# Performance work log

Measured on AMD Instinct MI355X. Metric: run time of the kernel, lower is better.

## Reference

```python
import jax, jax.numpy as jnp
import numpy as np

P, Q, B = 256, 48, 16      # passage len, question len, batch
E, H = 300, 128            # word embed size, hidden size
D = E + 2 * H              # preprocess GRU input dim (word emb + bidir char emb)


def _gru_layer(xs, Wih, Whh, bih, bhh):
    """torch.nn.GRU single layer over time. xs: [T,B,in] -> [T,B,H]."""
    def step(h, x):
        gi = x @ Wih.T + bih
        gh = h @ Whh.T + bhh
        ir, iz, inn = jnp.split(gi, 3, axis=-1)
        hr, hz, hn = jnp.split(gh, 3, axis=-1)
        r = jax.nn.sigmoid(ir + hr)
        z = jax.nn.sigmoid(iz + hz)
        n = jnp.tanh(inn + r * hn)
        h2 = (1.0 - z) * n + z * h
        return h2, h2
    h0 = jnp.zeros((xs.shape[1], Whh.shape[-1]), xs.dtype)
    return jax.lax.scan(step, h0, xs)[1]


def _lstm_cell(x, h, c, Wih, Whh, b):
    """torch.nn.LSTMCell gate order i,f,g,o."""
    g = x @ Wih.T + h @ Whh.T + b
    i, f, gg, o = jnp.split(g, 4, axis=-1)
    c2 = jax.nn.sigmoid(f) * c + jax.nn.sigmoid(i) * jnp.tanh(gg)
    return jax.nn.sigmoid(o) * jnp.tanh(c2), c2


def _preprocess(x, gru):
    """3-layer GRU run on forward and time-reversed input (shared weights), concat -> [T,B,2H]."""
    def run(xs):
        h = xs
        for (Wih, Whh, bih, bhh) in gru:
            h = _gru_layer(h, Wih, Whh, bih, bhh)
        return h
    Hf = run(x)
    Hb = jnp.flip(run(jnp.flip(x, 0)), 0)
    return jnp.concatenate([Hf, Hb], axis=-1)


def _bidir_attn_lstm(Hseq, Hmem, Wmem, Wcur, Whid, w_att, Wg, Wih, Whh, b):
    """Gated additive-attention LSTM (match-LSTM / self-matching) run in both
    directions over Hseq with a shared cell, attending over Hmem. -> [T,B,2H]."""
    att_mem = jnp.einsum('qbd,hd->qbh', Hmem, Wmem)          # [Tm,B,H], precomputed
    def step(carry, x_t):
        h, c = carry
        g = jnp.tanh(att_mem + x_t @ Wcur.T + h @ Whid.T)    # [Tm,B,H]
        a = jax.nn.softmax(jnp.einsum('qbh,h->qb', g, w_att), axis=0)
        w = jnp.einsum('qb,qbd->bd', a, Hmem)                # [B,2H]
        z = jnp.concatenate([x_t, w], axis=-1)               # [B,4H]
        z = z * jax.nn.sigmoid(z @ Wg.T)                     # gated attention input
        h, c = _lstm_cell(z, h, c, Wih, Whh, b)
        return (h, c), h
    z0 = jnp.zeros((Hseq.shape[1], Whh.shape[-1]), Hseq.dtype)
    Hf = jax.lax.scan(step, (z0, z0), Hseq)[1]
    Hb = jax.lax.scan(step, (z0, z0), jnp.flip(Hseq, 0))[1]
    return jnp.concatenate([Hf, jnp.flip(Hb, 0)], axis=-1)


def _forward(p_inp, q_inp, g0_Wih, g0_Whh, g0_bih, g0_bhh, g1_Wih, g1_Whh, g1_bih, g1_bhh, g2_Wih, g2_Whh, g2_bih, g2_bhh, Wq, Wp, Wh, w_alpha, Wg_m, m_Wih, m_Whh, m_b, Wsp, Wsh, w_gamma, Wg_s, s_Wih, s_Whh, s_b, Wal, Waa, w_beta, Wah, bah, Wac, bac, pt_Wih, pt_Whh, pt_b):
    gru = [(g0_Wih, g0_Whh, g0_bih, g0_bhh),
           (g1_Wih, g1_Whh, g1_bih, g1_bhh),
           (g2_Wih, g2_Whh, g2_bih, g2_bhh)]
    Hp = _preprocess(p_inp, gru)                             # [P,B,2H]
    Hq = _preprocess(q_inp, gru)                             # [Q,B,2H]
    # gated match-LSTM: passage attends over question
    Hr = _bidir_attn_lstm(Hp, Hq, Wq, Wp, Wh, w_alpha, Wg_m, m_Wih, m_Whh, m_b)
    # gated self-matching: passage attends over itself (shared attend_self_passage)
    Hs = _bidir_attn_lstm(Hr, Hr, Wsp, Wsp, Wsh, w_gamma, Wg_s, s_Wih, s_Whh, s_b)
    # answer pointer network, init state from pooled question representation
    qp = Hq.mean(axis=0)                                     # [B,2H]
    h = qp @ Wah.T + bah
    c = qp @ Wac.T + bac
    att = jnp.einsum('pbd,hd->pbh', Hs, Wal)                 # [P,B,H]
    betas = []
    for _ in range(2):                                       # start / end pointer steps
        g = jnp.tanh(att + h @ Waa.T)
        beta = jax.nn.softmax(jnp.einsum('pbh,h->pb', g, w_beta), axis=0)
        betas.append(beta)
        wv = jnp.einsum('pb,pbd->bd', beta, Hs)              # [B,2H]
        h, c = _lstm_cell(wv, h, c, pt_Wih, pt_Whh, pt_b)
    return jnp.stack(betas)                                  # [2,P,B]


def setup_inputs() -> dict:
    ks = iter(jax.random.split(jax.random.key(0), 64))
    def rn(shape, s=0.08):
        return jax.random.normal(next(ks), shape, jnp.float32) * s
    d = {}
    d['p_inp'] = jax.random.normal(next(ks), (P, B, D), jnp.float32)
    d['q_inp'] = jax.random.normal(next(ks), (Q, B, D), jnp.float32)
    for i, ind in enumerate([D, H, H]):
        d['g%d_Wih' % i] = rn((3 * H, ind))
        d['g%d_Whh' % i] = rn((3 * H, H))
        d['g%d_bih' % i] = jnp.zeros((3 * H,), jnp.float32)
        d['g%d_bhh' % i] = jnp.zeros((3 * H,), jnp.float32)
    d['Wq'] = rn((H, 2 * H)); d['Wp'] = rn((H, 2 * H)); d['Wh'] = rn((H, H))
    d['w_alpha'] = rn((H,))
    d['Wg_m'] = rn((4 * H, 4 * H))
    d['m_Wih'] = rn((4 * H, 4 * H)); d['m_Whh'] = rn((4 * H, H)); d['m_b'] = jnp.zeros((4 * H,), jnp.float32)
    d['Wsp'] = rn((H, 2 * H)); d['Wsh'] = rn((H, H)); d['w_gamma'] = rn((H,))
    d['Wg_s'] = rn((4 * H, 4 * H))
    d['s_Wih'] = rn((4 * H, 4 * H)); d['s_Whh'] = rn((4 * H, H)); d['s_b'] = jnp.zeros((4 * H,), jnp.float32)
    d['Wal'] = rn((H, 2 * H)); d['Waa'] = rn((H, H)); d['w_beta'] = rn((H,))
    d['Wah'] = rn((H, 2 * H)); d['bah'] = jnp.zeros((H,), jnp.float32)
    d['Wac'] = rn((H, 2 * H)); d['bac'] = jnp.zeros((H,), jnp.float32)
    d['pt_Wih'] = rn((4 * H, 2 * H)); d['pt_Whh'] = rn((4 * H, H)); d['pt_b'] = jnp.zeros((4 * H,), jnp.float32)
    return d


def reference(p_inp, q_inp, g0_Wih, g0_Whh, g0_bih, g0_bhh, g1_Wih, g1_Whh, g1_bih, g1_bhh, g2_Wih, g2_Whh, g2_bih, g2_bhh, Wq, Wp, Wh, w_alpha, Wg_m, m_Wih, m_Whh, m_b, Wsp, Wsh, w_gamma, Wg_s, s_Wih, s_Whh, s_b, Wal, Waa, w_beta, Wah, bah, Wac, bac, pt_Wih, pt_Whh, pt_b):
    return _forward(p_inp, q_inp, g0_Wih, g0_Whh, g0_bih, g0_bhh, g1_Wih, g1_Whh, g1_bih, g1_bhh, g2_Wih, g2_Whh, g2_bih, g2_bhh, Wq, Wp, Wh, w_alpha, Wg_m, m_Wih, m_Whh, m_b, Wsp, Wsh, w_gamma, Wg_s, s_Wih, s_Whh, s_b, Wal, Waa, w_beta, Wah, bah, Wac, bac, pt_Wih, pt_Whh, pt_b)
```

## Files before the change

kernel.cpp:

```cpp
#include <hip/hip_runtime.h>


#define PP 256
#define QQ 48
#define BB 16

typedef _Float16 f16;
typedef f16 f16x4 __attribute__((ext_vector_type(4)));
typedef f16 f16x8 __attribute__((ext_vector_type(8)));
typedef f16 h2 __attribute__((ext_vector_type(2)));

__device__ __forceinline__ float fast_rcp(float x) { return __builtin_amdgcn_rcpf(x); }
__device__ __forceinline__ float tanh_f(float x) {
  float e = __expf(2.0f * x);
  return 1.0f - 2.0f * fast_rcp(1.0f + e);
}
__device__ __forceinline__ float sigm_f(float x) {
  return fast_rcp(1.0f + __expf(-x));
}
__device__ __forceinline__ float fdot2(h2 a, h2 b, float c) {
#if defined(__has_builtin)
#if __has_builtin(__builtin_amdgcn_fdot2)
  return __builtin_amdgcn_fdot2(a, b, c, false);
#else
  return c + (float)a.x*(float)b.x + (float)a.y*(float)b.y;
#endif
#else
  return c + (float)a.x*(float)b.x + (float)a.y*(float)b.y;
#endif
}

__global__ __launch_bounds__(256) void gemm_nt(
    const float* __restrict__ A, int lda,
    const float* __restrict__ W, int ldw,
    const float* __restrict__ bias,
    float* __restrict__ C, int ldc, int K) {
  __shared__ float As[64][17];
  __shared__ float Ws[64][17];
  int tid = threadIdx.x;
  int m0 = blockIdx.x * 64, n0 = blockIdx.y * 64;
  int lr = tid >> 2, lq = (tid & 3) * 4;
  int tr = tid >> 4, tc = tid & 15;
  float acc[4][4] = {};
  for (int k0 = 0; k0 < K; k0 += 16) {
    float4 av = {0,0,0,0}, wv = {0,0,0,0};
    if (k0 + lq < K) {
      av = *(const float4*)&A[(size_t)(m0 + lr) * lda + k0 + lq];
      wv = *(const float4*)&W[(size_t)(n0 + lr) * ldw + k0 + lq];
    }
    __syncthreads();
    As[lr][lq+0] = av.x; As[lr][lq+1] = av.y; As[lr][lq+2] = av.z; As[lr][lq+3] = av.w;
    Ws[lr][lq+0] = wv.x; Ws[lr][lq+1] = wv.y; Ws[lr][lq+2] = wv.z; Ws[lr][lq+3] = wv.w;
    __syncthreads();
#pragma unroll
    for (int kk = 0; kk < 16; ++kk) {
      float a4[4], b4[4];
#pragma unroll
      for (int i = 0; i < 4; ++i) a4[i] = As[tr*4+i][kk];
#pragma unroll
      for (int j = 0; j < 4; ++j) b4[j] = Ws[tc*4+j][kk];
#pragma unroll
      for (int i = 0; i < 4; ++i)
#pragma unroll
        for (int j = 0; j < 4; ++j) acc[i][j] += a4[i] * b4[j];
    }
  }
#pragma unroll
  for (int i = 0; i < 4; ++i) {
    int m = m0 + tr*4 + i;
#pragma unroll
    for (int j = 0; j < 4; ++j) {
      int n = n0 + tc*4 + j;
      C[(size_t)m * ldc + n] = acc[i][j] + (bias ? bias[n] : 0.0f);
    }
  }
}

__global__ __launch_bounds__(256) void gemm_f16u(
    const float* __restrict__ A, int lda,
    const float* __restrict__ W, int ldw,
    f16* __restrict__ dst, int QMd, int K) {
  __shared__ float As[64][17];
  __shared__ float Ws[64][17];
  int tid = threadIdx.x;
  int m0 = blockIdx.x * 64, n0 = blockIdx.y * 64;
  int lr = tid >> 2, lq = (tid & 3) * 4;
  int tr = tid >> 4, tc = tid & 15;
  float acc[4][4] = {};
  for (int k0 = 0; k0 < K; k0 += 16) {
    float4 av = *(const float4*)&A[(size_t)(m0 + lr) * lda + k0 + lq];
    float4 wv = *(const float4*)&W[(size_t)(n0 + lr) * ldw + k0 + lq];
    __syncthreads();
    As[lr][lq+0] = av.x; As[lr][lq+1] = av.y; As[lr][lq+2] = av.z; As[lr][lq+3] = av.w;
    Ws[lr][lq+0] = wv.x; Ws[lr][lq+1] = wv.y; Ws[lr][lq+2] = wv.z; Ws[lr][lq+3] = wv.w;
    __syncthreads();
#pragma unroll
    for (int kk = 0; kk < 16; ++kk) {
      float a4[4], b4[4];
#pragma unroll
      for (int i = 0; i < 4; ++i) a4[i] = As[tr*4+i][kk];
#pragma unroll
      for (int j = 0; j < 4; ++j) b4[j] = Ws[tc*4+j][kk];
#pragma unroll
      for (int i = 0; i < 4; ++i)
#pragma unroll
        for (int j = 0; j < 4; ++j) acc[i][j] += a4[i] * b4[j];
    }
  }
#pragma unroll
  for (int i = 0; i < 4; ++i) {
    int m = m0 + tr*4 + i;
    int q = m >> 4, bb = m & 15;
#pragma unroll
    for (int j = 0; j < 4; ++j) {
      int n = n0 + tc*4 + j;
      dst[((size_t)bb*QMd + q)*768 + 256 + n] = (f16)acc[i][j];
    }
  }
}

__global__ void conv_hmemU(const float* __restrict__ src, f16* __restrict__ dst, int QM) {
  int q = blockIdx.x, b = blockIdx.y, d = threadIdx.x;
  dst[((size_t)b*QM + q)*768 + d] = (f16)src[((size_t)q*BB + b)*256 + d];
}

struct TDesc { const float* src; float* dst; int R, C, ld, off; };
struct TDescs { TDesc d[5]; };

__global__ __launch_bounds__(256) void transpose_many(TDescs ds) {
  TDesc d = ds.d[blockIdx.y];
  int idx = blockIdx.x * 256 + threadIdx.x;
  if (idx < d.R * d.C) {
    int r = idx / d.C, cc = idx % d.C;
    d.dst[(size_t)cc * d.R + r] = d.src[(size_t)r * d.ld + d.off + cc];
  }
}

struct HDesc { const float* src; f16* dst; int R, C, ld; };
struct HDescs { HDesc d[7]; };

__global__ __launch_bounds__(256) void conv_w16_many(HDescs ds) {
  HDesc d = ds.d[blockIdx.y];
  int idx = blockIdx.x * 256 + threadIdx.x;
  if (idx < d.R * d.C) {
    int j = idx / d.C, k = idx % d.C;
    d.dst[(size_t)k * d.R + j] = (f16)d.src[(size_t)j * d.ld + k];
  }
}

struct QDesc { const float* src; h2* dst; int J, K, ld; };
struct QDescs { QDesc d[2]; };

__global__ __launch_bounds__(256) void pack_pairs_many(QDescs ds) {
  QDesc d = ds.d[blockIdx.y];
  int KP = d.K >> 1;
  int idx = blockIdx.x * 256 + threadIdx.x;
  if (idx < KP * d.J) {
    int kp = idx / d.J, j = idx % d.J;
    h2 v;
    v.x = (f16)d.src[(size_t)j*d.ld + 2*kp];
    v.y = (f16)d.src[(size_t)j*d.ld + 2*kp + 1];
    d.dst[(size_t)kp*d.J + j] = v;
  }
}

__global__ __launch_bounds__(256) void conv_attT(
    const float* __restrict__ src, f16* __restrict__ dst, int QM) {
  int idx = blockIdx.x * 256 + threadIdx.x;
  if (idx < 16*128*QM) {
    int q = idx % QM, h = (idx / QM) & 127, b = idx / (QM*128);
    dst[idx] = (f16)src[((size_t)q*BB + b)*128 + h];
  }
}

__global__ __launch_bounds__(512) void gru_rec(
    const float* __restrict__ gi_p, const float* __restrict__ gi_q,
    const f16* __restrict__ WhhH,
    const float* __restrict__ bhh,
    float* __restrict__ out_p, float* __restrict__ out_q,
    float* __restrict__ Hp, float* __restrict__ Hq,
    int mode0, int finalmode) {
  int x = blockIdx.x;
  int seq = x >> 3, dir = (x >> 2) & 1, bg = x & 3;
  int T = seq ? QQ : PP;
  const float* gi = seq ? gi_q : gi_p;
  float* out = seq ? out_q : out_p;
  float* Hf  = seq ? Hq   : Hp;
  int b0 = bg * 4;
  int tid = threadIdx.x;
  __shared__ float hs[4][128];
  __shared__ float gpart[4][4][384];
  ((float*)hs)[tid] = 0.0f;
  __syncthreads();
  int ks = tid / 96;
  int jq = (tid % 96) * 4;
  int gb = tid >> 7, gj = tid & 127;
  for (int t = 0; t < T; ++t) {
    if (tid < 384) {
      float a[4][4] = {};
      const f16* wp = WhhH + (size_t)ks*32*384 + jq;
      const int kb = ks*32;
#pragma unroll 8
      for (int k = 0; k < 32; ++k) {
        f16x4 wv = *(const f16x4*)&wp[(size_t)k*384];
        float w0 = (float)wv[0], w1 = (float)wv[1], w2 = (float)wv[2], w3 = (float)wv[3];
#pragma unroll
        for (int bb = 0; bb < 4; ++bb) {
          float hv = hs[bb][kb + k];
          a[bb][0] += hv*w0; a[bb][1] += hv*w1; a[bb][2] += hv*w2; a[bb][3] += hv*w3;
        }
      }
#pragma unroll
      for (int bb = 0; bb < 4; ++bb) {
        gpart[ks][bb][jq+0]=a[bb][0]; gpart[ks][bb][jq+1]=a[bb][1];
        gpart[ks][bb][jq+2]=a[bb][2]; gpart[ks][bb][jq+3]=a[bb][3];
      }
    }
    __syncthreads();
    {
      size_t base;
      if (mode0) {
        int girow = dir ? (T-1-t) : t;
        base = ((size_t)girow*BB + b0+gb)*384;
      } else {
        base = (((size_t)dir*T + t)*BB + b0+gb)*384;
      }
      float ghr = bhh[gj]     + gpart[0][gb][gj]     + gpart[1][gb][gj]     + gpart[2][gb][gj]     + gpart[3][gb][gj];
      float ghz = bhh[128+gj] + gpart[0][gb][128+gj] + gpart[1][gb][128+gj] + gpart[2][gb][128+gj] + gpart[3][gb][128+gj];
      float ghn = bhh[256+gj] + gpart[0][gb][256+gj] + gpart[1][gb][256+gj] + gpart[2][gb][256+gj] + gpart[3][gb][256+gj];
      float gr = gi[base + gj], gz = gi[base + 128 + gj], gn = gi[base + 256 + gj];
      float r = sigm_f(gr + ghr);
      float z = sigm_f(gz + ghz);
      float n = tanh_f(gn + r * ghn);
      float h2v = (1.0f - z) * n + z * hs[gb][gj];
      hs[gb][gj] = h2v;
      if (finalmode) {
        int orow = dir ? (T-1-t) : t;
        Hf[((size_t)orow*BB + b0+gb)*256 + dir*128 + gj] = h2v;
      } else {
        out[(((size_t)dir*T + t)*BB + b0+gb)*128 + gj] = h2v;
      }
    }
    __syncthreads();
  }
}

template<int QM>
__global__ __launch_bounds__(512) void attn_rec2(
    const float* __restrict__ Hseq,
    const f16*  __restrict__ HmemU,
    const f16*  __restrict__ attT,
    const float* __restrict__ Xcur,
    const float* __restrict__ Xg,
    const float* __restrict__ watt,
    const f16*  __restrict__ WhidT,
    const h2*   __restrict__ WihP2,
    const f16*  __restrict__ WhhT,
    const float* __restrict__ bias,
    float* __restrict__ Hy) {
  constexpr bool HOST = (QM == QQ);
  constexpr int QP  = HOST ? 64 : 256;
  constexpr int HS  = 512 / QP;
  constexpr int hl  = 128 / HS;
  constexpr int hsh = HOST ? 6 : 8;
  constexpr int QR  = QM / 4;
  int dir = blockIdx.x >> 4, b = blockIdx.x & 15;
  int tid = threadIdx.x;
  __shared__ f16 attSL[HOST ? 128*QQ : 1];
  __shared__ f16 humSL[HOST ? QQ*768 : 1];
  __shared__ float h[128], c[128], xh[128], wa[128];
  __shared__ float peS[QP], zx[256];
  __shared__ h2 zgP[256];
  __shared__ float pA[4][128];
  __shared__ float pB[512];
  __shared__ float pDE[4][768];
  __shared__ float pG[8][512];
  __shared__ float biasS[512];
  __shared__ float red[1];
  if (tid < 128) { h[tid] = 0.0f; c[tid] = 0.0f; wa[tid] = watt[tid]; }
  biasS[tid] = bias[tid];
  const f16* attb = attT  + (size_t)b*128*QM;
  const f16* humb = HmemU + (size_t)b*QM*768;
  if constexpr (HOST) {
    for (int i = tid; i < QQ*768/8; i += 512)
      *(f16x8*)&humSL[i*8] = *(const f16x8*)&humb[(size_t)i*8];
    for (int i = tid; i < 128*QQ/8; i += 512)
      *(f16x8*)&attSL[i*8] = *(const f16x8*)&attb[(size_t)i*8];
  }
  __syncthreads();
  for (int t = 0; t < PP; ++t) {
    int row = dir ? (PP-1-t) : t;
    {
      int j = tid & 127, kh = tid >> 7;
      float acc = 0.0f;
      const f16* wp = WhidT + (size_t)kh*32*128 + j;
      const float* hp = &h[kh*32];
#pragma unroll
      for (int k = 0; k < 32; ++k) acc += (float)wp[(size_t)k*128] * hp[k];
      pA[kh][j] = acc;
      if (tid < 128) xh[tid] = Xcur[((size_t)row*BB + b)*128 + tid];
      else if (tid < 192) *(float4*)&zx[(tid-128)*4] =
          *(const float4*)&Hseq[((size_t)row*BB + b)*256 + (tid-128)*4];
    }
    __syncthreads();
    {
      int q = tid & (QP-1), hh = tid >> hsh;
      float acc = 0.0f;
      if (q < QM) {
        const f16* ap = (HOST ? attSL : attb) + q;
        int h0 = hh * hl;
#pragma unroll 8
        for (int i = 0; i < hl; ++i) {
          int h2i = h0 + i;
          float xv = xh[h2i] + pA[0][h2i] + pA[1][h2i] + pA[2][h2i] + pA[3][h2i];
          acc += wa[h2i] * tanh_f((float)ap[(size_t)h2i*QM] + xv);
        }
      }
      pB[hh*QP + q] = acc;
    }
    __syncthreads();
    if (tid < 64) {
      float lsum = 0.0f;
      for (int q2 = tid; q2 < QP; q2 += 64) {
        float s = 0.0f;
#pragma unroll
        for (int i = 0; i < HS; ++i) s += pB[i*QP + q2];
        float e = (q2 < QM) ? __expf(s) : 0.0f;
        peS[q2] = e; lsum += e;
      }
#pragma unroll
      for (int off = 32; off; off >>= 1) lsum += __shfl_down(lsum, off);
      if (tid == 0) red[0] = lsum;
    }
    __syncthreads();
    {
      int oc = tid & 127, qs = tid >> 7;
      if (oc < 96) {
        float a[8] = {};
        if constexpr (HOST) {
          const f16* hp = &humSL[(size_t)(qs*QR)*768 + oc*8];
#pragma unroll
          for (int i = 0; i < QR; ++i) {
            float pv = peS[qs*QR + i];
            f16x8 mv = *(const f16x8*)&hp[(size_t)i*768];
#pragma unroll
            for (int cN = 0; cN < 8; ++cN) a[cN] += pv * (float)mv[cN];
          }
        } else {
          const f16* hp = humb + (size_t)(qs*QR)*768 + oc*8;
#pragma unroll 16
          for (int i = 0; i < QR; ++i) {
            float pv = peS[qs*QR + i];
            f16x8 mv = *(const f16x8*)&hp[(size_t)i*768];
#pragma unroll
            for (int cN = 0; cN < 8; ++cN) a[cN] += pv * (float)mv[cN];
          }
        }
#pragma unroll
        for (int cN = 0; cN < 8; ++cN) pDE[qs][oc*8 + cN] = a[cN];
      }
    }
    __syncthreads();
    if (tid < 256) {
      float invd = fast_rcp(red[0]);
      int j0 = 2*tid;
      float u0 = (pDE[0][256+j0] + pDE[1][256+j0] + pDE[2][256+j0] + pDE[3][256+j0]) * invd;
      float u1 = (pDE[0][257+j0] + pDE[1][257+j0] + pDE[2][257+j0] + pDE[3][257+j0]) * invd;
      float z0, z1;
      if (tid < 128) { z0 = zx[j0]; z1 = zx[j0+1]; }
      else {
        int d0 = j0 - 256;
        z0 = (pDE[0][d0]   + pDE[1][d0]   + pDE[2][d0]   + pDE[3][d0])   * invd;
        z1 = (pDE[0][d0+1] + pDE[1][d0+1] + pDE[2][d0+1] + pDE[3][d0+1]) * invd;
      }
      float2 xg2 = *(const float2*)&Xg[((size_t)row*BB + b)*512 + j0];
      h2 p;
      p.x = (f16)(z0 * sigm_f(xg2.x + u0));
      p.y = (f16)(z1 * sigm_f(xg2.y + u1));
      zgP[tid] = p;
    }
    __syncthreads();
    {
      int jo = tid & 63, kh = tid >> 6;
      float a[8] = {};
      const h2* wp = WihP2 + (size_t)(kh*32)*512 + jo*8;
#pragma unroll 16
      for (int kp = 0; kp < 32; ++kp) {
        const f16* w8 = (const f16*)(wp + (size_t)kp*512);
        f16x8 wlo = *(const f16x8*)w8;
        f16x8 whi = *(const f16x8*)(w8 + 8);
        h2 zv = zgP[kh*32 + kp];
        h2 p0; p0.x = wlo[0]; p0.y = wlo[1];
        h2 p1; p1.x = wlo[2]; p1.y = wlo[3];
        h2 p2; p2.x = wlo[4]; p2.y = wlo[5];
        h2 p3; p3.x = wlo[6]; p3.y = wlo[7];
        h2 p4; p4.x = whi[0]; p4.y = whi[1];
        h2 p5; p5.x = whi[2]; p5.y = whi[3];
        h2 p6; p6.x = whi[4]; p6.y = whi[5];
        h2 p7; p7.x = whi[6]; p7.y = whi[7];
        a[0] = fdot2(p0, zv, a[0]); a[1] = fdot2(p1, zv, a[1]);
        a[2] = fdot2(p2, zv, a[2]); a[3] = fdot2(p3, zv, a[3]);
        a[4] = fdot2(p4, zv, a[4]); a[5] = fdot2(p5, zv, a[5]);
        a[6] = fdot2(p6, zv, a[6]); a[7] = fdot2(p7, zv, a[7]);
      }
      const f16* wp2 = WhhT + (size_t)(kh*16)*512 + jo*8;
      const float* hp = &h[kh*16];
#pragma unroll
      for (int k = 0; k < 16; ++k) {
        float hk = hp[k];
        f16x8 wv = *(const f16x8*)&wp2[(size_t)k*512];
#pragma unroll
        for (int cN = 0; cN < 8; ++cN) a[cN] += hk * (float)wv[cN];
      }
#pragma unroll
      for (int cN = 0; cN < 8; ++cN) pG[kh][jo*8 + cN] = a[cN];
    }
    __syncthreads();
    if (tid < 128) {
      float gi2 = biasS[tid], gf2 = biasS[128+tid], gg2 = biasS[256+tid], go2 = biasS[384+tid];
#pragma unroll
      for (int s = 0; s < 8; ++s) {
        gi2 += pG[s][tid];       gf2 += pG[s][128+tid];
        gg2 += pG[s][256+tid];   go2 += pG[s][384+tid];
      }
      float ii = sigm_f(gi2), ff = sigm_f(gf2), gg = tanh_f(gg2), oo = sigm_f(go2);
      float cn = ff * c[tid] + ii * gg;
      float hn = oo * tanh_f(cn);
      c[tid] = cn; h[tid] = hn;
      Hy[((size_t)row*BB + b)*256 + dir*128 + tid] = hn;
    }
    __syncthreads();
  }
}

__global__ __launch_bounds__(256) void ptr_net(
    const float* __restrict__ Hq,
    const float* __restrict__ Hs,
    const float* __restrict__ attp,
    const float* __restrict__ WaaT,
    const float* __restrict__ wbeta,
    const float* __restrict__ WahT,
    const float* __restrict__ bah,
    const float* __restrict__ WacT,
    const float* __restrict__ bac,
    const float* __restrict__ WihT,
    const float* __restrict__ WhhT,
    const float* __restrict__ bptr,
    float* __restrict__ out) {
  int b = blockIdx.x;
  int tid = threadIdx.x;
  __shared__ float qp[256], h[128], c[128], haa[128], pe2[256], wv[256], part[1024];
  __shared__ float red[1];
  {
    float acc = 0.0f;
#pragma unroll 8
    for (int q = 0; q < QQ; ++q) acc += Hq[((size_t)q*BB + b)*256 + tid];
    qp[tid] = acc * (1.0f/48.0f);
  }
  __syncthreads();
  if (tid < 128) {
    float ah = bah[tid], ac = bac[tid];
#pragma unroll 8
    for (int k = 0; k < 256; ++k) {
      ah += qp[k] * WahT[k*128 + tid];
      ac += qp[k] * WacT[k*128 + tid];
    }
    h[tid] = ah; c[tid] = ac;
  }
  __syncthreads();
  for (int step = 0; step < 2; ++step) {
    if (tid < 128) {
      float acc = 0.0f;
#pragma unroll 8
      for (int k = 0; k < 128; ++k) acc += h[k] * WaaT[k*128 + tid];
      haa[tid] = acc;
    }
    __syncthreads();
    {
      const float* ap = attp + (size_t)tid*BB*128 + b*128;
      float s = 0.0f;
#pragma unroll 8
      for (int k = 0; k < 128; ++k) s += wbeta[k] * tanh_f(ap[k] + haa[k]);
      pe2[tid] = __expf(s);
    }
    __syncthreads();
    if (tid < 64) {
      float s2 = pe2[tid] + pe2[tid+64] + pe2[tid+128] + pe2[tid+192];
#pragma unroll
      for (int off = 32; off; off >>= 1) s2 += __shfl_down(s2, off);
      if (tid == 0) red[0] = s2;
    }
    __syncthreads();
    float inv = fast_rcp(red[0]);
    out[((size_t)step*PP + tid)*BB + b] = pe2[tid] * inv;
    {
      float acc = 0.0f;
#pragma unroll 8
      for (int p2 = 0; p2 < PP; ++p2) acc += pe2[p2] * Hs[((size_t)p2*BB + b)*256 + tid];
      wv[tid] = acc * inv;
    }
    __syncthreads();
    {
      int jq = tid & 127, kh = tid >> 7;
      float a0=0,a1=0,a2=0,a3=0;
      const float* wp = WihT + (size_t)kh*128*512 + jq*4;
      const float* vp = &wv[kh*128];
#pragma unroll 16
      for (int k = 0; k < 128; ++k) {
        float4 w4 = *(const float4*)&wp[(size_t)k*512];
        float v = vp[k];
        a0 += v*w4.x; a1 += v*w4.y; a2 += v*w4.z; a3 += v*w4.w;
      }
      const float* wp2 = WhhT + (size_t)kh*64*512 + jq*4;
      const float* hp = &h[kh*64];
#pragma unroll
      for (int k = 0; k < 64; ++k) {
        float4 w4 = *(const float4*)&wp2[(size_t)k*512];
        float v = hp[k];
        a0 += v*w4.x; a1 += v*w4.y; a2 += v*w4.z; a3 += v*w4.w;
      }
      part[kh*512 + jq*4 + 0] = a0; part[kh*512 + jq*4 + 1] = a1;
      part[kh*512 + jq*4 + 2] = a2; part[kh*512 + jq*4 + 3] = a3;
    }
    __syncthreads();
    if (tid < 128) {
      float gii = bptr[tid]     + part[tid]     + part[512+tid];
      float gff = bptr[128+tid] + part[128+tid] + part[640+tid];
      float ggg = bptr[256+tid] + part[256+tid] + part[768+tid];
      float goo = bptr[384+tid] + part[384+tid] + part[896+tid];
      float ii = sigm_f(gii), ff = sigm_f(gff), gg = tanh_f(ggg), oo = sigm_f(goo);
      float cn = ff * c[tid] + ii * gg;
      h[tid] = oo * tanh_f(cn); c[tid] = cn;
    }
    __syncthreads();
  }
}

extern "C" void kernel_launch(void* const* d_in, const int* in_sizes, int n_in,
                              void* d_out, int out_size, void* d_ws, size_t ws_size,
                              hipStream_t stream) {
  const float* p_inp  = (const float*)d_in[0];
  const float* q_inp  = (const float*)d_in[1];
  const float* g0_Wih = (const float*)d_in[2];
  const float* g0_Whh = (const float*)d_in[3];
  const float* g0_bih = (const float*)d_in[4];
  const float* g0_bhh = (const float*)d_in[5];
  const float* g1_Wih = (const float*)d_in[6];
  const float* g1_Whh = (const float*)d_in[7];
  const float* g1_bih = (const float*)d_in[8];
  const float* g1_bhh = (const float*)d_in[9];
  const float* g2_Wih = (const float*)d_in[10];
  const float* g2_Whh = (const float*)d_in[11];
  const float* g2_bih = (const float*)d_in[12];
  const float* g2_bhh = (const float*)d_in[13];
  const float* Wq     = (const float*)d_in[14];
  const float* Wp     = (const float*)d_in[15];
  const float* Wh     = (const float*)d_in[16];
  const float* w_alpha= (const float*)d_in[17];
  const float* Wg_m   = (const float*)d_in[18];
  const float* m_Wih  = (const float*)d_in[19];
  const float* m_Whh  = (const float*)d_in[20];
  const float* m_b    = (const float*)d_in[21];
  const float* Wsp    = (const float*)d_in[22];
  const float* Wsh    = (const float*)d_in[23];
  const float* w_gamma= (const float*)d_in[24];
  const float* Wg_s   = (const float*)d_in[25];
  const float* s_Wih  = (const float*)d_in[26];
  const float* s_Whh  = (const float*)d_in[27];
  const float* s_b    = (const float*)d_in[28];
  const float* Wal    = (const float*)d_in[29];
  const float* Waa    = (const float*)d_in[30];
  const float* w_beta = (const float*)d_in[31];
  const float* Wah    = (const float*)d_in[32];
  const float* bah    = (const float*)d_in[33];
  const float* Wac    = (const float*)d_in[34];
  const float* bac    = (const float*)d_in[35];
  const float* pt_Wih = (const float*)d_in[36];
  const float* pt_Whh = (const float*)d_in[37];
  const float* pt_b   = (const float*)d_in[38];

  float* ws = (float*)d_ws;
  size_t o = 0;
  auto alloc = [&](size_t n) { float* p = ws + o; o += n; return p; };
  float* WaaT   = alloc(16384);
  float* WahT   = alloc(32768);
  float* WacT   = alloc(32768);
  float* ptWihT = alloc(131072);
  float* ptWhhT = alloc(65536);
  f16* g0WhhH = (f16*)alloc(24576);
  f16* g1WhhH = (f16*)alloc(24576);
  f16* g2WhhH = (f16*)alloc(24576);
  h2*  mWihP2 = (h2*)alloc(131072);
  f16* mWhhT  = (f16*)alloc(32768);
  f16* mWhidT = (f16*)alloc(8192);
  h2*  sWihP2 = (h2*)alloc(131072);
  f16* sWhhT  = (f16*)alloc(32768);
  f16* sWhidT = (f16*)alloc(8192);
  float* Hp  = alloc(1048576);
  float* Hq_ = alloc(196608);
  float* Hr  = alloc(1048576);
  float* Hs_ = alloc(1048576);
  float* A = alloc(6225920);
  float* gi_p = A;
  float* gi_q = A + 3145728;
  float* hA_p = A + 3735552;
  float* hB_p = A + 4784128;
  float* hA_q = A + 5832704;
  float* hB_q = A + 6029312;
  float* attq   = A;
  float* Xp     = A + 98304;
  float* XgM    = A + 622592;
  f16*   attqTH = (f16*)(A + 2719744);
  f16*   HqU16  = (f16*)(A + 2768896);
  float* XgS     = A;
  float* attsp   = A + 2097152;
  f16*   attspTH = (f16*)(A + 2621440);
  f16*   HrU16   = (f16*)(A + 2883584);
  float* attp = A;

  TDescs tds;
  tds.d[0] = { Waa,    WaaT,   128, 128, 128, 0 };
  tds.d[1] = { Wah,    WahT,   128, 256, 256, 0 };
  tds.d[2] = { Wac,    WacT,   128, 256, 256, 0 };
  tds.d[3] = { pt_Wih, ptWihT, 512, 256, 256, 0 };
  tds.d[4] = { pt_Whh, ptWhhT, 512, 128, 128, 0 };
  transpose_many<<<dim3(512, 5), 256, 0, stream>>>(tds);

  HDescs hds;
  hds.d[0] = { g0_Whh, g0WhhH, 384, 128, 128 };
  hds.d[1] = { g1_Whh, g1WhhH, 384, 128, 128 };
  hds.d[2] = { g2_Whh, g2WhhH, 384, 128, 128 };
  hds.d[3] = { m_Whh,  mWhhT,  512, 128, 128 };
  hds.d[4] = { Wh,     mWhidT, 128, 128, 128 };
  hds.d[5] = { s_Whh,  sWhhT,  512, 128, 128 };
  hds.d[6] = { Wsh,    sWhidT, 128, 128, 128 };
  conv_w16_many<<<dim3(256, 7), 256, 0, stream>>>(hds);

  QDescs qds;
  qds.d[0] = { m_Wih, mWihP2, 512, 512, 512 };
  qds.d[1] = { s_Wih, sWihP2, 512, 512, 512 };
  pack_pairs_many<<<dim3(512, 2), 256, 0, stream>>>(qds);

  gemm_nt<<<dim3(64, 6),  256, 0, stream>>>(p_inp, 556, g0_Wih, 556, g0_bih, gi_p, 384, 556);
  gemm_nt<<<dim3(12, 6),  256, 0, stream>>>(q_inp, 556, g0_Wih, 556, g0_bih, gi_q, 384, 556);
  gru_rec<<<16, 512, 0, stream>>>(gi_p, gi_q, g0WhhH, g0_bhh, hA_p, hA_q, nullptr, nullptr, 1, 0);
  gemm_nt<<<dim3(128, 6), 256, 0, stream>>>(hA_p, 128, g1_Wih, 128, g1_bih, gi_p, 384, 128);
  gemm_nt<<<dim3(24, 6),  256, 0, stream>>>(hA_q, 128, g1_Wih, 128, g1_bih, gi_q, 384, 128);
  gru_rec<<<16, 512, 0, stream>>>(gi_p, gi_q, g1WhhH, g1_bhh, hB_p, hB_q, nullptr, nullptr, 0, 0);
  gemm_nt<<<dim3(128, 6), 256, 0, stream>>>(hB_p, 128, g2_Wih, 128, g2_bih, gi_p, 384, 128);
  gemm_nt<<<dim3(24, 6),  256, 0, stream>>>(hB_q, 128, g2_Wih, 128, g2_bih, gi_q, 384, 128);
  gru_rec<<<16, 512, 0, stream>>>(gi_p, gi_q, g2WhhH, g2_bhh, hA_p, hA_q, Hp, Hq_, 0, 1);

  gemm_nt<<<dim3(12, 2), 256, 0, stream>>>(Hq_, 256, Wq, 256, nullptr, attq, 128, 256);
  gemm_nt<<<dim3(64, 2), 256, 0, stream>>>(Hp, 256, Wp, 256, nullptr, Xp, 128, 256);
  gemm_nt<<<dim3(64, 8), 256, 0, stream>>>(Hp, 256, Wg_m, 512, nullptr, XgM, 512, 256);
  gemm_f16u<<<dim3(12, 8), 256, 0, stream>>>(Hq_, 256, Wg_m + 256, 512, HqU16, QQ, 256);
  conv_hmemU<<<dim3(48, 16), 256, 0, stream>>>(Hq_, HqU16, 48);
  conv_attT<<<dim3(384), 256, 0, stream>>>(attq, attqTH, 48);
  attn_rec2<QQ><<<32, 512, 0, stream>>>(Hp, HqU16, attqTH, Xp, XgM, w_alpha,
                                        mWhidT, mWihP2, mWhhT, m_b, Hr);

  gemm_nt<<<dim3(64, 2), 256, 0, stream>>>(Hr, 256, Wsp, 256, nullptr, attsp, 128, 256);
  gemm_nt<<<dim3(64, 8), 256, 0, stream>>>(Hr, 256, Wg_s, 512, nullptr, XgS, 512, 256);
  gemm_f16u<<<dim3(64, 8), 256, 0, stream>>>(Hr, 256, Wg_s + 256, 512, HrU16, PP, 256);
  conv_hmemU<<<dim3(256, 16), 256, 0, stream>>>(Hr, HrU16, 256);
  conv_attT<<<dim3(2048), 256, 0, stream>>>(attsp, attspTH, 256);
  attn_rec2<PP><<<32, 512, 0, stream>>>(Hr, HrU16, attspTH, attsp, XgS, w_gamma,
                                        sWhidT, sWihP2, sWhhT, s_b, Hs_);

  gemm_nt<<<dim3(64, 2), 256, 0, stream>>>(Hs_, 256, Wal, 256, nullptr, attp, 128, 256);
  ptr_net<<<16, 256, 0, stream>>>(Hq_, Hs_, attp, WaaT, w_beta, WahT, bah, WacT, bac,
                                  ptWihT, ptWhhT, pt_b, (float*)d_out);
}
```

Baseline: 9.312 ms.

## Widen attention recurrence to 1024 threads and stage weights in LDS

The attention LSTM recurrence kernel now runs with 1024 threads per block. Every reduction stage (hidden projection, query-softmax partials, weighted memory sum, gate GEMV) is split over twice as many threads, and a separate pre-sum of the hidden projection is added. The attention key matrix is now staged in shared memory for both memory lengths, and the GRU recurrence caches its recurrent weight matrix in LDS once. The aim is to cut per-timestep latency on these serial recurrences. The cost is an extra barrier per step and much larger LDS use, which could fail to fit or limit occupancy.

```diff
diff --git a/kernel.cpp b/kernel.cpp
--- a/kernel.cpp
+++ b/kernel.cpp
@@ -173,7 +173,7 @@
   }
 }
 
-__global__ __launch_bounds__(512) void gru_rec(
+__global__ __launch_bounds__(512, 1) void gru_rec(
     const float* __restrict__ gi_p, const float* __restrict__ gi_q,
     const f16* __restrict__ WhhH,
     const float* __restrict__ bhh,
@@ -188,9 +188,12 @@
   float* Hf  = seq ? Hq   : Hp;
   int b0 = bg * 4;
   int tid = threadIdx.x;
+  __shared__ f16 whhS[128*384];
   __shared__ float hs[4][128];
   __shared__ float gpart[4][4][384];
-  ((float*)hs)[tid] = 0.0f;
+  for (int i = tid; i < 128*384/8; i += 512)
+    *(f16x8*)&whhS[i*8] = *(const f16x8*)&WhhH[(size_t)i*8];
+  if (tid < 256) { ((float*)hs)[tid] = 0.0f; ((float*)hs)[256+tid] = 0.0f; }
   __syncthreads();
   int ks = tid / 96;
   int jq = (tid % 96) * 4;
@@ -198,7 +201,7 @@
   for (int t = 0; t < T; ++t) {
     if (tid < 384) {
       float a[4][4] = {};
-      const f16* wp = WhhH + (size_t)ks*32*384 + jq;
+      const f16* wp = whhS + (size_t)ks*32*384 + jq;
       const int kb = ks*32;
 #pragma unroll 8
       for (int k = 0; k < 32; ++k) {
@@ -246,7 +249,7 @@
 }
 
 template<int QM>
-__global__ __launch_bounds__(512) void attn_rec2(
+__global__ __launch_bounds__(1024, 1) void attn_rec3(
     const float* __restrict__ Hseq,
     const f16*  __restrict__ HmemU,
     const f16*  __restrict__ attT,
@@ -260,32 +263,32 @@
     float* __restrict__ Hy) {
   constexpr bool HOST = (QM == QQ);
   constexpr int QP  = HOST ? 64 : 256;
-  constexpr int HS  = 512 / QP;
+  constexpr int HS  = 1024 / QP;
   constexpr int hl  = 128 / HS;
   constexpr int hsh = HOST ? 6 : 8;
-  constexpr int QR  = QM / 4;
+  constexpr int QR  = QM / 8;
   int dir = blockIdx.x >> 4, b = blockIdx.x & 15;
   int tid = threadIdx.x;
-  __shared__ f16 attSL[HOST ? 128*QQ : 1];
-  __shared__ f16 humSL[HOST ? QQ*768 : 1];
-  __shared__ float h[128], c[128], xh[128], wa[128];
+  __shared__ f16 attSL[128*QM];
+  __shared__ f16 humSL[HOST ? QQ*768 : 8];
+  __shared__ float h[128], c[128], xh[128], xc[128], wa[128];
   __shared__ float peS[QP], zx[256];
   __shared__ h2 zgP[256];
-  __shared__ float pA[4][128];
-  __shared__ float pB[512];
-  __shared__ float pDE[4][768];
+  __shared__ float pA[8][128];
+  __shared__ float pB[1024];
+  __shared__ float pDE[8][768];
   __shared__ float pG[8][512];
   __shared__ float biasS[512];
   __shared__ float red[1];
   if (tid < 128) { h[tid] = 0.0f; c[tid] = 0.0f; wa[tid] = watt[tid]; }
-  biasS[tid] = bias[tid];
+  if (tid < 512) biasS[tid] = bias[tid];
   const f16* attb = attT  + (size_t)b*128*QM;
   const f16* humb = HmemU + (size_t)b*QM*768;
+  for (int i = tid; i < 128*QM/8; i += 1024)
+    *(f16x8*)&attSL[i*8] = *(const f16x8*)&attb[(size_t)i*8];
   if constexpr (HOST) {
-    for (int i = tid; i < QQ*768/8; i += 512)
+    for (int i = tid; i < QQ*768/8; i += 1024)
       *(f16x8*)&humSL[i*8] = *(const f16x8*)&humb[(size_t)i*8];
-    for (int i = tid; i < 128*QQ/8; i += 512)
-      *(f16x8*)&attSL[i*8] = *(const f16x8*)&attb[(size_t)i*8];
   }
   __syncthreads();
   for (int t = 0; t < PP; ++t) {
@@ -293,27 +296,33 @@
     {
       int j = tid & 127, kh = tid >> 7;
       float acc = 0.0f;
-      const f16* wp = WhidT + (size_t)kh*32*128 + j;
-      const float* hp = &h[kh*32];
-#pragma unroll
-      for (int k = 0; k < 32; ++k) acc += (float)wp[(size_t)k*128] * hp[k];
+      const f16* wp = WhidT + (size_t)kh*16*128 + j;
+      const float* hp = &h[kh*16];
+#pragma unroll
+      for (int k = 0; k < 16; ++k) acc += (float)wp[(size_t)k*128] * hp[k];
       pA[kh][j] = acc;
-      if (tid < 128) xh[tid] = Xcur[((size_t)row*BB + b)*128 + tid];
+      if (tid < 128) xc[tid] = Xcur[((size_t)row*BB + b)*128 + tid];
       else if (tid < 192) *(float4*)&zx[(tid-128)*4] =
           *(const float4*)&Hseq[((size_t)row*BB + b)*256 + (tid-128)*4];
+    }
+    __syncthreads();
+    if (tid < 128) {
+      float a = xc[tid];
+#pragma unroll
+      for (int i = 0; i < 8; ++i) a += pA[i][tid];
+      xh[tid] = a;
     }
     __syncthreads();
     {
       int q = tid & (QP-1), hh = tid >> hsh;
       float acc = 0.0f;
       if (q < QM) {
-        const f16* ap = (HOST ? attSL : attb) + q;
+        const f16* ap = attSL + q;
         int h0 = hh * hl;
 #pragma unroll 8
         for (int i = 0; i < hl; ++i) {
-          int h2i = h0 + i;
-          float xv = xh[h2i] + pA[0][h2i] + pA[1][h2i] + pA[2][h2i] + pA[3][h2i];
-          acc += wa[h2i] * tanh_f((float)ap[(size_t)h2i*QM] + xv);
+          int hx = h0 + i;
+          acc += wa[hx] * tanh_f((float)ap[(size_t)hx*QM] + xh[hx]);
         }
       }
       pB[hh*QP + q] = acc;
@@ -348,7 +357,7 @@
           }
         } else {
           const f16* hp = humb + (size_t)(qs*QR)*768 + oc*8;
-#pragma unroll 16
+#pragma unroll 8
           for (int i = 0; i < QR; ++i) {
             float pv = peS[qs*QR + i];
             f16x8 mv = *(const f16x8*)&hp[(size_t)i*768];
@@ -364,14 +373,18 @@
     if (tid < 256) {
       float invd = fast_rcp(red[0]);
       int j0 = 2*tid;
-      float u0 = (pDE[0][256+j0] + pDE[1][256+j0] + pDE[2][256+j0] + pDE[3][256+j0]) * invd;
-      float u1 = (pDE[0][257+j0] + pDE[1][257+j0] + pDE[2][257+j0] + pDE[3][257+j0]) * invd;
+      float u0 = 0.0f, u1 = 0.0f;
+#pragma unroll
+      for (int s = 0; s < 8; ++s) { u0 += pDE[s][256+j0]; u1 += pDE[s][257+j0]; }
+      u0 *= invd; u1 *= invd;
       float z0, z1;
       if (tid < 128) { z0 = zx[j0]; z1 = zx[j0+1]; }
       else {
         int d0 = j0 - 256;
-        z0 = (pDE[0][d0]   + pDE[1][d0]   + pDE[2][d0]   + pDE[3][d0])   * invd;
-        z1 = (pDE[0][d0+1] + pDE[1][d0+1] + pDE[2][d0+1] + pDE[3][d0+1]) * invd;
+        float w0 = 0.0f, w1 = 0.0f;
+#pragma unroll
+        for (int s = 0; s < 8; ++s) { w0 += pDE[s][d0]; w1 += pDE[s][d0+1]; }
+        z0 = w0 * invd; z1 = w1 * invd;
       }
       float2 xg2 = *(const float2*)&Xg[((size_t)row*BB + b)*512 + j0];
       h2 p;
@@ -381,39 +394,30 @@
     }
     __syncthreads();
     {
-      int jo = tid & 63, kh = tid >> 6;
-      float a[8] = {};
-      const h2* wp = WihP2 + (size_t)(kh*32)*512 + jo*8;
-#pragma unroll 16
+      int jo = tid & 127, kh = tid >> 7;
+      float a0=0,a1=0,a2=0,a3=0;
+      const h2* wp = WihP2 + (size_t)(kh*32)*512 + jo*4;
+#pragma unroll 8
       for (int kp = 0; kp < 32; ++kp) {
-        const f16* w8 = (const f16*)(wp + (size_t)kp*512);
-        f16x8 wlo = *(const f16x8*)w8;
-        f16x8 whi = *(const f16x8*)(w8 + 8);
+        f16x8 wv = *(const f16x8*)(const f16*)(wp + (size_t)kp*512);
         h2 zv = zgP[kh*32 + kp];
-        h2 p0; p0.x = wlo[0]; p0.y = wlo[1];
-        h2 p1; p1.x = wlo[2]; p1.y = wlo[3];
-        h2 p2; p2.x = wlo[4]; p2.y = wlo[5];
-        h2 p3; p3.x = wlo[6]; p3.y = wlo[7];
-        h2 p4; p4.x = whi[0]; p4.y = whi[1];
-        h2 p5; p5.x = whi[2]; p5.y = whi[3];
-        h2 p6; p6.x = whi[4]; p6.y = whi[5];
-        h2 p7; p7.x = whi[6]; p7.y = whi[7];
-        a[0] = fdot2(p0, zv, a[0]); a[1] = fdot2(p1, zv, a[1]);
-        a[2] = fdot2(p2, zv, a[2]); a[3] = fdot2(p3, zv, a[3]);
-        a[4] = fdot2(p4, zv, a[4]); a[5] = fdot2(p5, zv, a[5]);
-        a[6] = fdot2(p6, zv, a[6]); a[7] = fdot2(p7, zv, a[7]);
-      }
-      const f16* wp2 = WhhT + (size_t)(kh*16)*512 + jo*8;
+        h2 p0; p0.x = wv[0]; p0.y = wv[1];
+        h2 p1; p1.x = wv[2]; p1.y = wv[3];
+        h2 p2; p2.x = wv[4]; p2.y = wv[5];
+        h2 p3; p3.x = wv[6]; p3.y = wv[7];
+        a0 = fdot2(p0, zv, a0); a1 = fdot2(p1, zv, a1);
+        a2 = fdot2(p2, zv, a2); a3 = fdot2(p3, zv, a3);
+      }
+      const f16* wp2 = WhhT + (size_t)(kh*16)*512 + jo*4;
       const float* hp = &h[kh*16];
 #pragma unroll
       for (int k = 0; k < 16; ++k) {
         float hk = hp[k];
-        f16x8 wv = *(const f16x8*)&wp2[(size_t)k*512];
-#pragma unroll
-        for (int cN = 0; cN < 8; ++cN) a[cN] += hk * (float)wv[cN];
-      }
-#pragma unroll
-      for (int cN = 0; cN < 8; ++cN) pG[kh][jo*8 + cN] = a[cN];
+        f16x4 wv = *(const f16x4*)&wp2[(size_t)k*512];
+        a0 += hk*(float)wv[0]; a1 += hk*(float)wv[1];
+        a2 += hk*(float)wv[2]; a3 += hk*(float)wv[3];
+      }
+      pG[kh][jo*4+0]=a0; pG[kh][jo*4+1]=a1; pG[kh][jo*4+2]=a2; pG[kh][jo*4+3]=a3;
     }
     __syncthreads();
     if (tid < 128) {
@@ -657,16 +661,16 @@
   gemm_f16u<<<dim3(12, 8), 256, 0, stream>>>(Hq_, 256, Wg_m + 256, 512, HqU16, QQ, 256);
   conv_hmemU<<<dim3(48, 16), 256, 0, stream>>>(Hq_, HqU16, 48);
   conv_attT<<<dim3(384), 256, 0, stream>>>(attq, attqTH, 48);
-  attn_rec2<QQ><<<32, 512, 0, stream>>>(Hp, HqU16, attqTH, Xp, XgM, w_alpha,
-                                        mWhidT, mWihP2, mWhhT, m_b, Hr);
+  attn_rec3<QQ><<<32, 1024, 0, stream>>>(Hp, HqU16, attqTH, Xp, XgM, w_alpha,
+                                         mWhidT, mWihP2, mWhhT, m_b, Hr);
 
   gemm_nt<<<dim3(64, 2), 256, 0, stream>>>(Hr, 256, Wsp, 256, nullptr, attsp, 128, 256);
   gemm_nt<<<dim3(64, 8), 256, 0, stream>>>(Hr, 256, Wg_s, 512, nullptr, XgS, 512, 256);
   gemm_f16u<<<dim3(64, 8), 256, 0, stream>>>(Hr, 256, Wg_s + 256, 512, HrU16, PP, 256);
   conv_hmemU<<<dim3(256, 16), 256, 0, stream>>>(Hr, HrU16, 256);
   conv_attT<<<dim3(2048), 256, 0, stream>>>(attsp, attspTH, 256);
-  attn_rec2<PP><<<32, 512, 0, stream>>>(Hr, HrU16, attspTH, attsp, XgS, w_gamma,
-                                        sWhidT, sWihP2, sWhhT, s_b, Hs_);
+  attn_rec3<PP><<<32, 1024, 0, stream>>>(Hr, HrU16, attspTH, attsp, XgS, w_gamma,
+                                         sWhidT, sWihP2, sWhhT, s_b, Hs_);
 
   gemm_nt<<<dim3(64, 2), 256, 0, stream>>>(Hs_, 256, Wal, 256, nullptr, attp, 128, 256);
   ptr_net<<<16, 256, 0, stream>>>(Hq_, Hs_, attp, WaaT, w_beta, WahT, bah, WacT, bac,
```

Result: faster. 8.674 ms (-6.8%).
